# Performance work log

Hardware: AMD Instinct MI355X
Metric: run time of the kernel (lower is better)

## Reference

```python
import jax, jax.numpy as jnp
import numpy as np

D_MODEL = 2048
D_FF = 8192


def _act_quant(x):
    # BitNet b1.58 per-token int8 absmax activation quantization with STE passthrough
    scale = 127.0 / jnp.clip(jnp.max(jnp.abs(x), axis=-1, keepdims=True), 1e-5)
    xq = jnp.clip(jnp.round(x * scale), -128.0, 127.0) / scale
    return x + jax.lax.stop_gradient(xq - x)


def _weight_quant(w):
    # Ternary {-1,0,1} weight quantization with per-tensor mean-abs scale
    scale = 1.0 / jnp.clip(jnp.mean(jnp.abs(w)), 1e-5)
    wq = jnp.clip(jnp.round(w * scale), -1.0, 1.0) / scale
    return w + jax.lax.stop_gradient(wq - w)


def _bitlinear(x, w):
    # y = Q_act(x) @ Q_w(w)^T   (w has shape [out, in], torch Linear convention)
    return jnp.einsum('bsd,fd->bsf', _act_quant(x), _weight_quant(w))


def setup_inputs() -> dict:
    key = jax.random.key(0)
    k_x, k_w1, k_w2 = jax.random.split(key, 3)
    x = jax.random.normal(k_x, (4, 4096, D_MODEL), dtype=jnp.float32)
    # torch Linear default init scale ~ 1/sqrt(fan_in)
    W1 = jax.random.normal(k_w1, (D_FF, D_MODEL), dtype=jnp.float32) / np.sqrt(D_MODEL)
    W2 = jax.random.normal(k_w2, (D_MODEL, D_FF), dtype=jnp.float32) / np.sqrt(D_FF)
    return {"x": x, "W1": W1, "W2": W2}


def reference(x, W1, W2):
    h = jax.nn.silu(_bitlinear(x, W1))   # [B, S, d_ff]
    return _bitlinear(h, W2)             # [B, S, d_model]; dropout p=0 -> identity
```

## Files before the change

kernel.cpp:

```cpp
#include <hip/hip_runtime.h>
#include <hip/hip_bf16.h>
#include <cstdint>

#define DM 2048
#define DF 8192

typedef int v4i __attribute__((ext_vector_type(4)));
typedef short v8s __attribute__((ext_vector_type(8)));

__device__ __forceinline__ float silu_f(float y) {
  return y * (1.0f / (1.0f + expf(-y)));
}

__device__ __forceinline__ void gload_lds16(const void* g, void* l) {
  __builtin_amdgcn_global_load_lds(
      (const __attribute__((address_space(1))) void*)g,
      (__attribute__((address_space(3))) void*)l, 16, 0, 0);
}

__global__ __launch_bounds__(256) void abs_sum_k(const float* __restrict__ w,
                                                 float* __restrict__ partial) {
  const int t = threadIdx.x;
  const float4* wp = (const float4*)w;
  const long base = (long)blockIdx.x * 4096;
  float s = 0.f;
#pragma unroll
  for (int i = 0; i < 16; ++i) {
    float4 v = wp[base + i * 256 + t];
    s += fabsf(v.x) + fabsf(v.y) + fabsf(v.z) + fabsf(v.w);
  }
#pragma unroll
  for (int d = 1; d < 64; d <<= 1) s += __shfl_xor(s, d, 64);
  __shared__ float wsum[4];
  if ((t & 63) == 0) wsum[t >> 6] = s;
  __syncthreads();
  if (t == 0) partial[blockIdx.x] = (wsum[0] + wsum[1]) + (wsum[2] + wsum[3]);
}

__global__ __launch_bounds__(256) void finalize_scales_k(const float* __restrict__ p1,
                                                         const float* __restrict__ p2,
                                                         float* __restrict__ sc) {
  const float* p = (blockIdx.x == 0) ? p1 : p2;
  const int t = threadIdx.x;
  float s = (p[t] + p[t + 256]) + (p[t + 512] + p[t + 768]);
#pragma unroll
  for (int d = 1; d < 64; d <<= 1) s += __shfl_xor(s, d, 64);
  __shared__ float wsum[4];
  if ((t & 63) == 0) wsum[t >> 6] = s;
  __syncthreads();
  if (t == 0) {
    float total = (wsum[0] + wsum[1]) + (wsum[2] + wsum[3]);
    float mean = total * (1.0f / 16777216.0f);
    float c = fmaxf(mean, 1e-5f);
    sc[blockIdx.x * 2 + 0] = 1.0f / c;
    sc[blockIdx.x * 2 + 1] = c;
  }
}

__global__ __launch_bounds__(256) void tern_quant_k(const float* __restrict__ w,
                                                    int8_t* __restrict__ wq,
                                                    const float* __restrict__ scp) {
  const float s = scp[0];
  const long i = (long)blockIdx.x * 256 + threadIdx.x;
  float4 v = ((const float4*)w)[i];
  int q0 = (int)rintf(v.x * s); q0 = q0 < -1 ? -1 : (q0 > 1 ? 1 : q0);
  int q1 = (int)rintf(v.y * s); q1 = q1 < -1 ? -1 : (q1 > 1 ? 1 : q1);
  int q2 = (int)rintf(v.z * s); q2 = q2 < -1 ? -1 : (q2 > 1 ? 1 : q2);
  int q3 = (int)rintf(v.w * s); q3 = q3 < -1 ? -1 : (q3 > 1 ? 1 : q3);
  ((int*)wq)[i] = (q0 & 255) | ((q1 & 255) << 8) | ((q2 & 255) << 16) | ((q3 & 255) << 24);
}

__global__ __launch_bounds__(256) void act_quant_x_k(const float* __restrict__ x,
                                                     int8_t* __restrict__ xq,
                                                     float* __restrict__ inv_sx) {
  const int t = threadIdx.x;
  const long row = blockIdx.x;
  const float4* xr = (const float4*)(x + row * DM);
  float4 v0 = xr[t * 2], v1 = xr[t * 2 + 1];
  float m = fmaxf(fmaxf(fmaxf(fabsf(v0.x), fabsf(v0.y)), fmaxf(fabsf(v0.z), fabsf(v0.w))),
                  fmaxf(fmaxf(fabsf(v1.x), fabsf(v1.y)), fmaxf(fabsf(v1.z), fabsf(v1.w))));
#pragma unroll
  for (int d = 1; d < 64; d <<= 1) m = fmaxf(m, __shfl_xor(m, d, 64));
  __shared__ float wm[4];
  if ((t & 63) == 0) wm[t >> 6] = m;
  __syncthreads();
  m = fmaxf(fmaxf(wm[0], wm[1]), fmaxf(wm[2], wm[3]));
  const float scale = 127.0f / fmaxf(m, 1e-5f);
  if (t == 0) inv_sx[row] = 1.0f / scale;
  float vv[8] = {v0.x, v0.y, v0.z, v0.w, v1.x, v1.y, v1.z, v1.w};
  int q[8];
#pragma unroll
  for (int j = 0; j < 8; ++j) {
    int qq = (int)rintf(vv[j] * scale);
    q[j] = qq < -128 ? -128 : (qq > 127 ? 127 : qq);
  }
  int lo = (q[0] & 255) | ((q[1] & 255) << 8) | ((q[2] & 255) << 16) | ((q[3] & 255) << 24);
  int hi = (q[4] & 255) | ((q[5] & 255) << 8) | ((q[6] & 255) << 16) | ((q[7] & 255) << 24);
  ((int2*)(xq + row * DM))[t] = make_int2(lo, hi);
}

template <int MO, int NO>
__device__ __forceinline__ void cluster(const v4i (&af)[4][2], const v4i (&bf)[2][2],
                                        v4i (&acc)[8][4]) {
  __builtin_amdgcn_s_setprio(1);
#pragma unroll
  for (int ks = 0; ks < 2; ++ks)
#pragma unroll
    for (int m = 0; m < 4; ++m)
#pragma unroll
      for (int n = 0; n < 2; ++n)
        acc[MO + m][NO + n] = __builtin_amdgcn_mfma_i32_16x16x64_i8(
            af[m][ks], bf[n][ks], acc[MO + m][NO + n], 0, 0, 0);
  __builtin_amdgcn_s_setprio(0);
}

template <int K, int N, int EPI>
__global__ __launch_bounds__(512, 2) void gemm8_i8_k(
    const int8_t* __restrict__ A, const int8_t* __restrict__ B,
    const float* __restrict__ rowInv, const float* __restrict__ invswp,
    short* __restrict__ Y16, float* __restrict__ Out) {
  constexpr int NT = K / 128;
  constexpr int NBX = N / 256;
  __shared__ __align__(16) uint8_t lds[131072];

  const int t = threadIdx.x;
  const int wave = t >> 6;
  const int lane = t & 63;
  const int wr = wave >> 2;
  const int wc = wave & 3;
  const int l15 = lane & 15, l4 = lane >> 4;

  const int cpx = (int)gridDim.x >> 3;
  const int bid0 = blockIdx.x;
  const int bid = (bid0 & 7) * cpx + (bid0 >> 3);
  const int bx = bid % NBX, by = bid / NBX;
  const long arow0 = (long)by * 256;
  const long bcol0 = (long)bx * 256;

  const int8_t* Ablk = A + arow0 * K;
  const int8_t* Bblk = B + bcol0 * K;

  const int srow = t >> 3;
  const int scol = ((t & 7) ^ (srow & 7)) << 4;

  const int rAo = (wr * 128 + l15) * 128;
  const int rBo = (wc * 64 + l15) * 128;
  const int sw = (l15 & 7) << 4;
  const int cc0 = (l4 * 16) ^ sw;
  const int cc1 = (64 | (l4 * 16)) ^ sw;

  v4i acc[8][4] = {};
  v4i a_lo[4][2], a_hi[4][2], b_lo[2][2], b_hi[2][2];

#define STAGE(ktile_, part_)                                                      \
  do {                                                                            \
    const int kk = (ktile_);                                                      \
    if (kk < NT) {                                                                \
      uint8_t* d0 = lds + ((kk & 1) << 16) + ((part_) << 14) + (wave << 10);      \
      const int8_t* sp = ((part_) < 2) ? Ablk : Bblk;                             \
      const int8_t* s0 =                                                          \
          sp + (long)((((part_) & 1) << 7) + srow) * K + ((long)kk << 7) + scol;  \
      gload_lds16(s0, d0);                                                        \
      gload_lds16(s0 + ((long)K << 6), d0 + 8192);                                \
    }                                                                             \
  } while (0)

#define LGKM0 asm volatile("s_waitcnt lgkmcnt(0)" ::: "memory"); \
              __builtin_amdgcn_sched_barrier(0)
#define SB    __builtin_amdgcn_sched_barrier(0)

  STAGE(0, 0); STAGE(0, 1); STAGE(0, 2); STAGE(0, 3);
  STAGE(1, 0); STAGE(1, 1);
  asm volatile("s_waitcnt vmcnt(4)" ::: "memory");
  __builtin_amdgcn_s_barrier();

  for (int kt = 0; kt < NT; ++kt) {
    const uint8_t* sA = lds + ((kt & 1) << 16);
    const uint8_t* sB = sA + 32768;

#pragma unroll
    for (int m = 0; m < 4; ++m) {
      a_lo[m][0] = *(const v4i*)(sA + rAo + m * 2048 + cc0);
      a_lo[m][1] = *(const v4i*)(sA + rAo + m * 2048 + cc1);
    }
#pragma unroll
    for (int n = 0; n < 2; ++n) {
      b_lo[n][0] = *(const v4i*)(sB + rBo + n * 2048 + cc0);
      b_lo[n][1] = *(const v4i*)(sB + rBo + n * 2048 + cc1);
    }
    STAGE(kt + 1, 2);
    LGKM0;
#pragma unroll
    for (int m = 0; m < 4; ++m) {
      a_hi[m][0] = *(const v4i*)(sA + rAo + (m + 4) * 2048 + cc0);
      a_hi[m][1] = *(const v4i*)(sA + rAo + (m + 4) * 2048 + cc1);
    }
    STAGE(kt + 1, 3);
    SB;
    cluster<0, 0>(a_lo, b_lo, acc);
    LGKM0;
#pragma unroll
    for (int n = 0; n < 2; ++n) {
      b_hi[n][0] = *(const v4i*)(sB + rBo + (n + 2) * 2048 + cc0);
      b_hi[n][1] = *(const v4i*)(sB + rBo + (n + 2) * 2048 + cc1);
    }
    __builtin_amdgcn_s_barrier();
    STAGE(kt + 2, 0);
    SB;
    cluster<4, 0>(a_hi, b_lo, acc);
    LGKM0;
    STAGE(kt + 2, 1);
    SB;
    cluster<0, 2>(a_lo, b_hi, acc);
    cluster<4, 2>(a_hi, b_hi, acc);
    if (kt < NT - 2) {
      asm volatile("s_waitcnt vmcnt(4)" ::: "memory");
    } else if (kt == NT - 2) {
      asm volatile("s_waitcnt vmcnt(0)" ::: "memory");
    }
    __builtin_amdgcn_s_barrier();
  }

  if constexpr (EPI == 1) {
    __syncthreads();
#pragma unroll
    for (int mi = 0; mi < 8; ++mi) {
#pragma unroll
      for (int r = 0; r < 4; ++r) {
        const int row = wr * 128 + mi * 16 + l4 * 4 + r;
#pragma unroll
        for (int ni = 0; ni < 4; ++ni) {
          int yi = acc[mi][ni][r];
          int ys = yi < -32767 ? -32767 : (yi > 32767 ? 32767 : yi);
          const int col = wc * 64 + ni * 16 + l15;
          *(short*)(lds + ((row * 512 + col * 2) ^ ((row & 7) << 4))) = (short)ys;
        }
      }
    }
    __syncthreads();
    const int row = t >> 1;
    const int half = t & 1;
    short* gp = Y16 + (arow0 + row) * (long)DF + bcol0 + half * 128;
#pragma unroll
    for (int i = 0; i < 16; ++i) {
      v8s yv = *(const v8s*)(lds + ((row * 512 + half * 256 + i * 16) ^ ((row & 7) << 4)));
      *(v8s*)(gp + i * 8) = yv;
    }
  } else {
    const float invsw = invswp[0];
#pragma unroll
    for (int mi = 0; mi < 8; ++mi) {
#pragma unroll
      for (int r = 0; r < 4; ++r) {
        const long grow = arow0 + wr * 128 + mi * 16 + l4 * 4 + r;
        const float c2 = rowInv[grow] * invsw;
#pragma unroll
        for (int ni = 0; ni < 4; ++ni)
          Out[grow * N + bcol0 + wc * 64 + ni * 16 + l15] = (float)acc[mi][ni][r] * c2;
      }
    }
  }
#undef STAGE
#undef LGKM0
#undef SB
}

__global__ __launch_bounds__(256) void quant_h_k(const short* __restrict__ Y16,
                                                 const float* __restrict__ inv_sx,
                                                 const float* __restrict__ sc,
                                                 int8_t* __restrict__ hq,
                                                 float* __restrict__ inv_sh) {
  const int t = threadIdx.x;
  const long row = blockIdx.x;
  const float c1 = inv_sx[row] * sc[1];
  const v8s* yp = (const v8s*)(Y16 + row * DF);
  float h[32];
  float mx = 0.f;
#pragma unroll
  for (int b = 0; b < 4; ++b) {
    v8s s8 = yp[b * 256 + t];
#pragma unroll
    for (int j = 0; j < 8; ++j) {
      float hv = silu_f((float)s8[j] * c1);
      h[b * 8 + j] = hv;
      mx = fmaxf(mx, fabsf(hv));
    }
  }
#pragma unroll
  for (int d = 1; d < 64; d <<= 1) mx = fmaxf(mx, __shfl_xor(mx, d, 64));
  __shared__ float wm[4];
  if ((t & 63) == 0) wm[t >> 6] = mx;
  __syncthreads();
  const float m = fmaxf(fmaxf(wm[0], wm[1]), fmaxf(wm[2], wm[3]));
  const float scale = 127.0f / fmaxf(m, 1e-5f);
  if (t == 0) inv_sh[row] = 1.0f / scale;
  int2* op = (int2*)(hq + row * DF);
#pragma unroll
  for (int b = 0; b < 4; ++b) {
    int q[8];
#pragma unroll
    for (int j = 0; j < 8; ++j) {
      int qq = (int)rintf(h[b * 8 + j] * scale);
      q[j] = qq < -128 ? -128 : (qq > 127 ? 127 : qq);
    }
    int lo = (q[0] & 255) | ((q[1] & 255) << 8) | ((q[2] & 255) << 16) | ((q[3] & 255) << 24);
    int hi = (q[4] & 255) | ((q[5] & 255) << 8) | ((q[6] & 255) << 16) | ((q[7] & 255) << 24);
    op[b * 256 + t] = make_int2(lo, hi);
  }
}

extern "C" void kernel_launch(void* const* d_in, const int* in_sizes, int n_in,
                              void* d_out, int out_size, void* d_ws, size_t ws_size,
                              hipStream_t stream) {
  const float* x = (const float*)d_in[0];
  const float* W1 = (const float*)d_in[1];
  const float* W2 = (const float*)d_in[2];
  float* out = (float*)d_out;

  uint8_t* w = (uint8_t*)d_ws;
  float* sc = (float*)(w + 0);
  float* p1 = (float*)(w + 256);
  float* p2 = (float*)(w + 256 + 4096);
  float* inv_sx = (float*)(w + 8448);
  float* inv_sh = (float*)(w + 8448 + 65536);
  uint8_t* w1q = w + 8448 + 131072 + 4194304;
  uint8_t* w2q = w1q + 16777216;
  uint8_t* xq = w2q + 16777216;
  uint8_t* hq = xq + 33554432;
  short* y16 = (short*)(hq + 134217728);

  abs_sum_k<<<1024, 256, 0, stream>>>(W1, p1);
  abs_sum_k<<<1024, 256, 0, stream>>>(W2, p2);
  finalize_scales_k<<<2, 256, 0, stream>>>(p1, p2, sc);
  tern_quant_k<<<16384, 256, 0, stream>>>(W1, (int8_t*)w1q, sc + 0);
  tern_quant_k<<<16384, 256, 0, stream>>>(W2, (int8_t*)w2q, sc + 2);
  act_quant_x_k<<<16384, 256, 0, stream>>>(x, (int8_t*)xq, inv_sx);
  gemm8_i8_k<2048, 8192, 1><<<2048, 512, 0, stream>>>(
      (const int8_t*)xq, (const int8_t*)w1q, nullptr, nullptr, y16, nullptr);
  quant_h_k<<<16384, 256, 0, stream>>>(y16, inv_sx, sc, (int8_t*)hq, inv_sh);
  gemm8_i8_k<8192, 2048, 0><<<512, 512, 0, stream>>>(
      (const int8_t*)hq, (const int8_t*)w2q, inv_sh, sc + 3, nullptr, out);
}
```

Baseline: 764.7 us.

## Software-pipeline LDS fragment loads in the int8 GEMM loop with partial lgkmcnt waits

Restructures the int8 MFMA main loop so the next tile's A-low fragments are preloaded from LDS before the current iteration's later MFMA clusters run. All B and A-high LDS reads are now issued up front. The full lgkmcnt(0) waits become graded lgkmcnt(12)/(8) waits, so MFMA clusters can start as soon as their operands arrive. The aim is to hide LDS read latency behind matrix math. The cost is more live registers and an extra vmcnt wait placed mid-iteration.

New measurement: 763.2 us. About the same (-0.2%).

```diff
diff --git a/kernel.cpp b/kernel.cpp
--- a/kernel.cpp
+++ b/kernel.cpp
@@ -165,58 +165,77 @@
     }                                                                             \
   } while (0)
 
-#define LGKM0 asm volatile("s_waitcnt lgkmcnt(0)" ::: "memory"); \
-              __builtin_amdgcn_sched_barrier(0)
-#define SB    __builtin_amdgcn_sched_barrier(0)
+#define SB __builtin_amdgcn_sched_barrier(0)
+#define WAIT_LGKM12 asm volatile("s_waitcnt lgkmcnt(12)" ::: "memory"); SB
+#define WAIT_LGKM8  asm volatile("s_waitcnt lgkmcnt(8)"  ::: "memory"); SB
+#define WAIT_LGKM0  asm volatile("s_waitcnt lgkmcnt(0)"  ::: "memory"); SB
+#define WAIT_VM4    asm volatile("s_waitcnt vmcnt(4)"    ::: "memory"); SB
+#define WAIT_VM0    asm volatile("s_waitcnt vmcnt(0)"    ::: "memory"); SB
 
   STAGE(0, 0); STAGE(0, 1); STAGE(0, 2); STAGE(0, 3);
   STAGE(1, 0); STAGE(1, 1);
-  asm volatile("s_waitcnt vmcnt(4)" ::: "memory");
+  WAIT_VM4;
   __builtin_amdgcn_s_barrier();
+  {
+    const uint8_t* sA0 = lds;
+#pragma unroll
+    for (int m = 0; m < 4; ++m) {
+      a_lo[m][0] = *(const v4i*)(sA0 + rAo + m * 2048 + cc0);
+      a_lo[m][1] = *(const v4i*)(sA0 + rAo + m * 2048 + cc1);
+    }
+  }
+  SB;
 
   for (int kt = 0; kt < NT; ++kt) {
     const uint8_t* sA = lds + ((kt & 1) << 16);
     const uint8_t* sB = sA + 32768;
-
-#pragma unroll
-    for (int m = 0; m < 4; ++m) {
-      a_lo[m][0] = *(const v4i*)(sA + rAo + m * 2048 + cc0);
-      a_lo[m][1] = *(const v4i*)(sA + rAo + m * 2048 + cc1);
-    }
+    const uint8_t* sAn = lds + (((kt + 1) & 1) << 16);
+
 #pragma unroll
     for (int n = 0; n < 2; ++n) {
       b_lo[n][0] = *(const v4i*)(sB + rBo + n * 2048 + cc0);
       b_lo[n][1] = *(const v4i*)(sB + rBo + n * 2048 + cc1);
     }
-    STAGE(kt + 1, 2);
-    LGKM0;
+    SB;
+#pragma unroll
+    for (int n = 0; n < 2; ++n) {
+      b_hi[n][0] = *(const v4i*)(sB + rBo + (n + 2) * 2048 + cc0);
+      b_hi[n][1] = *(const v4i*)(sB + rBo + (n + 2) * 2048 + cc1);
+    }
+    SB;
 #pragma unroll
     for (int m = 0; m < 4; ++m) {
       a_hi[m][0] = *(const v4i*)(sA + rAo + (m + 4) * 2048 + cc0);
       a_hi[m][1] = *(const v4i*)(sA + rAo + (m + 4) * 2048 + cc1);
     }
+    SB;
+    STAGE(kt + 1, 2);
     STAGE(kt + 1, 3);
     SB;
+    WAIT_LGKM12;
     cluster<0, 0>(a_lo, b_lo, acc);
-    LGKM0;
-#pragma unroll
-    for (int n = 0; n < 2; ++n) {
-      b_hi[n][0] = *(const v4i*)(sB + rBo + (n + 2) * 2048 + cc0);
-      b_hi[n][1] = *(const v4i*)(sB + rBo + (n + 2) * 2048 + cc1);
-    }
+    WAIT_LGKM8;
+    cluster<0, 2>(a_lo, b_hi, acc);
+    WAIT_VM4;
+    WAIT_LGKM0;
     __builtin_amdgcn_s_barrier();
+    if (kt + 1 < NT) {
+#pragma unroll
+      for (int m = 0; m < 4; ++m) {
+        a_lo[m][0] = *(const v4i*)(sAn + rAo + m * 2048 + cc0);
+        a_lo[m][1] = *(const v4i*)(sAn + rAo + m * 2048 + cc1);
+      }
+      SB;
+    }
     STAGE(kt + 2, 0);
+    STAGE(kt + 2, 1);
     SB;
     cluster<4, 0>(a_hi, b_lo, acc);
-    LGKM0;
-    STAGE(kt + 2, 1);
-    SB;
-    cluster<0, 2>(a_lo, b_hi, acc);
     cluster<4, 2>(a_hi, b_hi, acc);
     if (kt < NT - 2) {
-      asm volatile("s_waitcnt vmcnt(4)" ::: "memory");
-    } else if (kt == NT - 2) {
-      asm volatile("s_waitcnt vmcnt(0)" ::: "memory");
+      WAIT_VM4;
+    } else {
+      WAIT_VM0;
     }
     __builtin_amdgcn_s_barrier();
   }
@@ -261,8 +280,12 @@
     }
   }
 #undef STAGE
-#undef LGKM0
 #undef SB
+#undef WAIT_LGKM12
+#undef WAIT_LGKM8
+#undef WAIT_LGKM0
+#undef WAIT_VM4
+#undef WAIT_VM0
 }
 
 __global__ __launch_bounds__(256) void quant_h_k(const short* __restrict__ Y16,
```

## Replace 256x256 8-wave int8 GEMM with 128x128 4-wave double-buffered kernel

Applied to the files above, without the earlier changes.

Both int8 GEMMs move from a 256x256 tile with 8 waves, 128KB LDS and an interleaved multi-part staging schedule to a 128x128 tile with 4 waves, 32KB LDS and a simple double buffer over K=64 slices. The smaller footprint permits four blocks per CU and a much larger grid, aiming for more occupancy and a simpler pipeline. In exchange, each loaded byte is reused less, so global/L2 traffic per FLOP grows, and each K step now ends in a full vmcnt(0) wait plus a barrier, exposing load latency.

New measurement: 943.3 us. 23.3% more time.

```diff
diff --git a/kernel.cpp b/kernel.cpp
--- a/kernel.cpp
+++ b/kernel.cpp
@@ -99,160 +99,113 @@
   ((int2*)(xq + row * DM))[t] = make_int2(lo, hi);
 }
 
-template <int MO, int NO>
-__device__ __forceinline__ void cluster(const v4i (&af)[4][2], const v4i (&bf)[2][2],
-                                        v4i (&acc)[8][4]) {
-  __builtin_amdgcn_s_setprio(1);
-#pragma unroll
-  for (int ks = 0; ks < 2; ++ks)
-#pragma unroll
-    for (int m = 0; m < 4; ++m)
-#pragma unroll
-      for (int n = 0; n < 2; ++n)
-        acc[MO + m][NO + n] = __builtin_amdgcn_mfma_i32_16x16x64_i8(
-            af[m][ks], bf[n][ks], acc[MO + m][NO + n], 0, 0, 0);
-  __builtin_amdgcn_s_setprio(0);
-}
-
 template <int K, int N, int EPI>
-__global__ __launch_bounds__(512, 2) void gemm8_i8_k(
+__global__ __launch_bounds__(256, 4) void gemm4w_i8_k(
     const int8_t* __restrict__ A, const int8_t* __restrict__ B,
     const float* __restrict__ rowInv, const float* __restrict__ invswp,
     short* __restrict__ Y16, float* __restrict__ Out) {
-  constexpr int NT = K / 128;
-  constexpr int NBX = N / 256;
-  __shared__ __align__(16) uint8_t lds[131072];
+  constexpr int NT = K / 64;
+  constexpr int NBX = N / 128;
+  __shared__ __align__(16) uint8_t lds[32768];
 
   const int t = threadIdx.x;
   const int wave = t >> 6;
   const int lane = t & 63;
-  const int wr = wave >> 2;
-  const int wc = wave & 3;
+  const int wr = wave >> 1;
+  const int wc = wave & 1;
   const int l15 = lane & 15, l4 = lane >> 4;
 
   const int cpx = (int)gridDim.x >> 3;
   const int bid0 = blockIdx.x;
   const int bid = (bid0 & 7) * cpx + (bid0 >> 3);
   const int bx = bid % NBX, by = bid / NBX;
-  const long arow0 = (long)by * 256;
-  const long bcol0 = (long)bx * 256;
-
-  const int8_t* Ablk = A + arow0 * K;
-  const int8_t* Bblk = B + bcol0 * K;
-
-  const int srow = t >> 3;
-  const int scol = ((t & 7) ^ (srow & 7)) << 4;
-
-  const int rAo = (wr * 128 + l15) * 128;
-  const int rBo = (wc * 64 + l15) * 128;
-  const int sw = (l15 & 7) << 4;
-  const int cc0 = (l4 * 16) ^ sw;
-  const int cc1 = (64 | (l4 * 16)) ^ sw;
-
-  v4i acc[8][4] = {};
-  v4i a_lo[4][2], a_hi[4][2], b_lo[2][2], b_hi[2][2];
-
-#define STAGE(ktile_, part_)                                                      \
-  do {                                                                            \
-    const int kk = (ktile_);                                                      \
-    if (kk < NT) {                                                                \
-      uint8_t* d0 = lds + ((kk & 1) << 16) + ((part_) << 14) + (wave << 10);      \
-      const int8_t* sp = ((part_) < 2) ? Ablk : Bblk;                             \
-      const int8_t* s0 =                                                          \
-          sp + (long)((((part_) & 1) << 7) + srow) * K + ((long)kk << 7) + scol;  \
-      gload_lds16(s0, d0);                                                        \
-      gload_lds16(s0 + ((long)K << 6), d0 + 8192);                                \
-    }                                                                             \
+  const long arow0 = (long)by * 128;
+  const long bcol0 = (long)bx * 128;
+
+  const int u0 = (t & 7) ^ ((t >> 3) & 7);
+  const int r0 = 2 * (t >> 3) + (u0 >> 2);
+  const int j0 = u0 & 3;
+  const int8_t* pA0 = A + (arow0 + r0) * (long)K + j0 * 16;
+  const int8_t* pA1 = pA0 + (long)64 * K;
+  const int8_t* pB0 = B + (bcol0 + r0) * (long)K + j0 * 16;
+  const int8_t* pB1 = pB0 + (long)64 * K;
+
+  const int lslot = ((((l15 & 1) << 2) | l4) ^ (l15 >> 1)) << 4;
+  const int rA = wr * 4096 + (l15 >> 1) * 128 + lslot;
+  const int rB = wc * 4096 + (l15 >> 1) * 128 + lslot;
+
+  v4i acc[4][4] = {};
+  v4i a[4], b[4];
+
+#define STAGE(kk)                                                   \
+  do {                                                              \
+    if ((kk) < NT) {                                                \
+      const long ko = ((long)(kk)) << 6;                            \
+      uint8_t* d = lds + (((kk) & 1) << 14);                        \
+      gload_lds16(pA0 + ko, d + t * 16);                            \
+      gload_lds16(pA1 + ko, d + 4096 + t * 16);                     \
+      gload_lds16(pB0 + ko, d + 8192 + t * 16);                     \
+      gload_lds16(pB1 + ko, d + 12288 + t * 16);                    \
+    }                                                               \
   } while (0)
 
-#define LGKM0 asm volatile("s_waitcnt lgkmcnt(0)" ::: "memory"); \
-              __builtin_amdgcn_sched_barrier(0)
-#define SB    __builtin_amdgcn_sched_barrier(0)
-
-  STAGE(0, 0); STAGE(0, 1); STAGE(0, 2); STAGE(0, 3);
-  STAGE(1, 0); STAGE(1, 1);
-  asm volatile("s_waitcnt vmcnt(4)" ::: "memory");
+  STAGE(0);
+  asm volatile("s_waitcnt vmcnt(0)" ::: "memory");
   __builtin_amdgcn_s_barrier();
 
   for (int kt = 0; kt < NT; ++kt) {
-    const uint8_t* sA = lds + ((kt & 1) << 16);
-    const uint8_t* sB = sA + 32768;
-
-#pragma unroll
-    for (int m = 0; m < 4; ++m) {
-      a_lo[m][0] = *(const v4i*)(sA + rAo + m * 2048 + cc0);
-      a_lo[m][1] = *(const v4i*)(sA + rAo + m * 2048 + cc1);
-    }
-#pragma unroll
-    for (int n = 0; n < 2; ++n) {
-      b_lo[n][0] = *(const v4i*)(sB + rBo + n * 2048 + cc0);
-      b_lo[n][1] = *(const v4i*)(sB + rBo + n * 2048 + cc1);
-    }
-    STAGE(kt + 1, 2);
-    LGKM0;
-#pragma unroll
-    for (int m = 0; m < 4; ++m) {
-      a_hi[m][0] = *(const v4i*)(sA + rAo + (m + 4) * 2048 + cc0);
-      a_hi[m][1] = *(const v4i*)(sA + rAo + (m + 4) * 2048 + cc1);
-    }
-    STAGE(kt + 1, 3);
-    SB;
-    cluster<0, 0>(a_lo, b_lo, acc);
-    LGKM0;
-#pragma unroll
-    for (int n = 0; n < 2; ++n) {
-      b_hi[n][0] = *(const v4i*)(sB + rBo + (n + 2) * 2048 + cc0);
-      b_hi[n][1] = *(const v4i*)(sB + rBo + (n + 2) * 2048 + cc1);
-    }
-    __builtin_amdgcn_s_barrier();
-    STAGE(kt + 2, 0);
-    SB;
-    cluster<4, 0>(a_hi, b_lo, acc);
-    LGKM0;
-    STAGE(kt + 2, 1);
-    SB;
-    cluster<0, 2>(a_lo, b_hi, acc);
-    cluster<4, 2>(a_hi, b_hi, acc);
-    if (kt < NT - 2) {
-      asm volatile("s_waitcnt vmcnt(4)" ::: "memory");
-    } else if (kt == NT - 2) {
-      asm volatile("s_waitcnt vmcnt(0)" ::: "memory");
-    }
+    const uint8_t* sAb = lds + ((kt & 1) << 14);
+    const uint8_t* sBb = sAb + 8192;
+#pragma unroll
+    for (int mi = 0; mi < 4; ++mi) a[mi] = *(const v4i*)(sAb + rA + mi * 1024);
+#pragma unroll
+    for (int ni = 0; ni < 4; ++ni) b[ni] = *(const v4i*)(sBb + rB + ni * 1024);
+    STAGE(kt + 1);
+    asm volatile("s_waitcnt lgkmcnt(0)" ::: "memory");
+    __builtin_amdgcn_sched_barrier(0);
+    __builtin_amdgcn_s_setprio(1);
+#pragma unroll
+    for (int mi = 0; mi < 4; ++mi)
+#pragma unroll
+      for (int ni = 0; ni < 4; ++ni)
+        acc[mi][ni] = __builtin_amdgcn_mfma_i32_16x16x64_i8(a[mi], b[ni], acc[mi][ni], 0, 0, 0);
+    __builtin_amdgcn_s_setprio(0);
+    asm volatile("s_waitcnt vmcnt(0)" ::: "memory");
     __builtin_amdgcn_s_barrier();
   }
 
   if constexpr (EPI == 1) {
     __syncthreads();
 #pragma unroll
-    for (int mi = 0; mi < 8; ++mi) {
+    for (int mi = 0; mi < 4; ++mi) {
 #pragma unroll
       for (int r = 0; r < 4; ++r) {
-        const int row = wr * 128 + mi * 16 + l4 * 4 + r;
+        const int row = wr * 64 + mi * 16 + l4 * 4 + r;
 #pragma unroll
         for (int ni = 0; ni < 4; ++ni) {
           int yi = acc[mi][ni][r];
           int ys = yi < -32767 ? -32767 : (yi > 32767 ? 32767 : yi);
           const int col = wc * 64 + ni * 16 + l15;
-          *(short*)(lds + ((row * 512 + col * 2) ^ ((row & 7) << 4))) = (short)ys;
+          *(short*)(lds + row * 256 + ((col * 2) ^ ((row & 7) << 4))) = (short)ys;
         }
       }
     }
     __syncthreads();
     const int row = t >> 1;
     const int half = t & 1;
-    short* gp = Y16 + (arow0 + row) * (long)DF + bcol0 + half * 128;
-#pragma unroll
-    for (int i = 0; i < 16; ++i) {
-      v8s yv = *(const v8s*)(lds + ((row * 512 + half * 256 + i * 16) ^ ((row & 7) << 4)));
+    short* gp = Y16 + (arow0 + row) * (long)DF + bcol0 + half * 64;
+#pragma unroll
+    for (int i = 0; i < 8; ++i) {
+      v8s yv = *(const v8s*)(lds + row * 256 + ((half * 128 + i * 16) ^ ((row & 7) << 4)));
       *(v8s*)(gp + i * 8) = yv;
     }
   } else {
     const float invsw = invswp[0];
 #pragma unroll
-    for (int mi = 0; mi < 8; ++mi) {
+    for (int mi = 0; mi < 4; ++mi) {
 #pragma unroll
       for (int r = 0; r < 4; ++r) {
-        const long grow = arow0 + wr * 128 + mi * 16 + l4 * 4 + r;
+        const long grow = arow0 + wr * 64 + mi * 16 + l4 * 4 + r;
         const float c2 = rowInv[grow] * invsw;
 #pragma unroll
         for (int ni = 0; ni < 4; ++ni)
@@ -261,8 +214,6 @@
     }
   }
 #undef STAGE
-#undef LGKM0
-#undef SB
 }
 
 __global__ __launch_bounds__(256) void quant_h_k(const short* __restrict__ Y16,
@@ -335,9 +286,9 @@
   tern_quant_k<<<16384, 256, 0, stream>>>(W1, (int8_t*)w1q, sc + 0);
   tern_quant_k<<<16384, 256, 0, stream>>>(W2, (int8_t*)w2q, sc + 2);
   act_quant_x_k<<<16384, 256, 0, stream>>>(x, (int8_t*)xq, inv_sx);
-  gemm8_i8_k<2048, 8192, 1><<<2048, 512, 0, stream>>>(
+  gemm4w_i8_k<2048, 8192, 1><<<8192, 256, 0, stream>>>(
       (const int8_t*)xq, (const int8_t*)w1q, nullptr, nullptr, y16, nullptr);
   quant_h_k<<<16384, 256, 0, stream>>>(y16, inv_sx, sc, (int8_t*)hq, inv_sh);
-  gemm8_i8_k<8192, 2048, 0><<<512, 512, 0, stream>>>(
+  gemm4w_i8_k<8192, 2048, 0><<<2048, 256, 0, stream>>>(
       (const int8_t*)hq, (const int8_t*)w2q, inv_sh, sc + 3, nullptr, out);
 }
```
